# Optimization experiments

Measured on AMD Instinct MI355X. Metric: run time of the kernel, lower is better.

## Reference

```python
import jax, jax.numpy as jnp
import numpy as np
from jax import lax

T = 256   # sequence length (hard-coded in source: tiled to 256 chars)
L = 128   # num_layers of each GRU stack


def _gru_stack(seq, w_ih, w_hh, b_ih, b_hh):
    """Multi-layer GRU with input_size=hidden_size=1 (torch gate order r,z,n).

    seq:  [T] scalar sequence (feature dim squeezed since H=in=1)
    w_ih, w_hh, b_ih, b_hh: [L, 3] stacked per-layer scalar weights/biases
    returns (out_seq [T], h_n [L])
    """
    def layer(carry_seq, params):
        wi, wh, bi, bh = params  # each [3]
        def step(h, xt):
            gi = wi * xt + bi            # [3] input gates
            gh = wh * h + bh             # [3] hidden gates
            r = jax.nn.sigmoid(gi[0] + gh[0])
            z = jax.nn.sigmoid(gi[1] + gh[1])
            n = jnp.tanh(gi[2] + r * gh[2])
            h_new = (1.0 - z) * n + z * h
            return h_new, h_new
        hT, out = lax.scan(step, jnp.zeros((), carry_seq.dtype), carry_seq)
        return out, hT
    out_seq, h_stack = lax.scan(layer, seq, (w_ih, w_hh, b_ih, b_hh))
    return out_seq, h_stack


def setup_inputs() -> dict:
    key = jax.random.key(0)
    ks = jax.random.split(key, 9)
    # torch GRU init: U(-1/sqrt(H), 1/sqrt(H)) = U(-1, 1) since H=1
    mk = lambda k: jax.random.uniform(k, (L, 3), jnp.float32, -1.0, 1.0)
    return {
        "X": jax.random.normal(ks[0], (T, 1), jnp.float32),
        "enc_w_ih": mk(ks[1]), "enc_w_hh": mk(ks[2]),
        "enc_b_ih": mk(ks[3]), "enc_b_hh": mk(ks[4]),
        "dec_w_ih": mk(ks[5]), "dec_w_hh": mk(ks[6]),
        "dec_b_ih": mk(ks[7]), "dec_b_hh": mk(ks[8]),
    }


def reference(X, enc_w_ih, enc_w_hh, enc_b_ih, enc_b_hh,
              dec_w_ih, dec_w_hh, dec_b_ih, dec_b_hh):
    seq = X[:, 0]  # [T]
    enc_out, _ = _gru_stack(seq, enc_w_ih, enc_w_hh, enc_b_ih, enc_b_hh)
    dec_out, dec_h = _gru_stack(enc_out, dec_w_ih, dec_w_hh, dec_b_ih, dec_b_hh)
    # training-mode return: decoder (output [T,1], h_n [L,1])
    return dec_out[:, None], dec_h[:, None]
```

## Files before the change

### kernel.cpp

```cpp
#include <hip/hip_runtime.h>


#define T_LEN 256
#define MBOX  320
typedef unsigned long long u64;
typedef unsigned int u32;

__device__ __forceinline__ float fexp2(float x) { return __builtin_amdgcn_exp2f(x); }
__device__ __forceinline__ float frcp(float x)  { return __builtin_amdgcn_rcpf(x); }

struct CellW {
    float wri, wrh, brc;
    float wzi, wzh, bzc;
    float wni, bni;
    float wnh, bnh;
};

__device__ __forceinline__ float cell_step(const CellW& c, float x, float h) {
    const float xr  = __builtin_fmaf(c.wri, x, c.brc);
    const float xz  = __builtin_fmaf(c.wzi, x, c.bzc);
    const float gin = __builtin_fmaf(c.wni, x, c.bni);
    const float ghn = __builtin_fmaf(c.wnh, h, c.bnh);
    const float er  = fexp2(__builtin_fmaf(c.wrh, h, xr));
    const float ez  = fexp2(__builtin_fmaf(c.wzh, h, xz));
    const float r   = frcp(1.0f + er);
    const float z   = frcp(1.0f + ez);
    const float en  = fexp2(__builtin_fmaf(r, ghn, gin));
    const float q   = frcp(1.0f + en);
    const float A   = __builtin_fmaf(z, h - 1.0f, 1.0f);
    const float B   = __builtin_fmaf(2.0f, z, -2.0f);
    return __builtin_fmaf(q, B, A);
}

template<bool LAST>
__device__ __forceinline__ float run_wave(
    const int j, const CellW& c,
    volatile u64* inbox, volatile u64* outbox,
    float* __restrict__ out, float* __restrict__ dumpG)
{
    float h = 0.0f;
    float hc_prev = 0.0f;
    u32 coll = 0;
    const int js = j & 7;

    {
        u64 v = inbox[8];
        while (__ballot((u32)(v >> 32) == 9u) != ~0ull) v = inbox[8];
    }

    for (int s0 = 0; s0 < 320; s0 += 8) {
        u32 bval = 0;
        if (s0 < T_LEN) {
            const int slot = s0 + js;
            u64 v = inbox[slot];
            while (__ballot((u32)(v >> 32) == (u32)(slot + 1)) != ~0ull)
                v = inbox[slot];
            bval = (u32)v;
        }
        #pragma unroll
        for (int si = 0; si < 8; ++si) {
            const int s = s0 + si;
            const int xv = __builtin_amdgcn_readlane((int)bval, si);
            const int xm = __builtin_amdgcn_update_dpp(
                xv, __builtin_bit_cast(int, hc_prev),
                0x138 , 0xF, 0xF, false);
            const float x = __builtin_bit_cast(float, xm);

            const float hc = cell_step(c, x, h);
            const int t = s - j;
            h = ((u32)t < (u32)T_LEN) ? hc : h;
            hc_prev = hc;

            const int cs = __builtin_amdgcn_update_dpp(
                0, (int)coll, 0x130 , 0xF, 0xF, false);
            coll = (j == 63) ? __builtin_bit_cast(u32, h) : (u32)cs;

            if (si == 6) {
                const int  tm   = s + j - 126;
                const bool real = (j >= 56) & (tm >= 0);
                const int  widx = real ? tm : (T_LEN + j);
                outbox[widx] = ((u64)(u32)(tm + 1) << 32) | (u64)coll;
                if (LAST) {
                    float* p = real ? (out + tm) : (dumpG + j);
                    *p = __builtin_bit_cast(float, coll);
                }
            }
        }
    }
    return h;
}

__global__ __launch_bounds__(256, 1) void gru_pipe8(
    const float* __restrict__ X,
    const float* __restrict__ enc_w_ih, const float* __restrict__ enc_w_hh,
    const float* __restrict__ enc_b_ih, const float* __restrict__ enc_b_hh,
    const float* __restrict__ dec_w_ih, const float* __restrict__ dec_w_hh,
    const float* __restrict__ dec_b_ih, const float* __restrict__ dec_b_hh,
    float* __restrict__ out, float* __restrict__ dumpG)
{
    const int tid = threadIdx.x;
    const int w   = tid >> 6;
    const int j   = tid & 63;

    __shared__ u64 xsM[T_LEN];
    __shared__ u64 box[4][MBOX];

    xsM[tid] = ((u64)(u32)(tid + 1) << 32) |
               (u64)__builtin_bit_cast(u32, X[tid]);
    box[0][tid] = 0ull;
    box[1][tid] = 0ull;
    box[2][tid] = 0ull;
    box[3][tid] = 0ull;

    const int pl = tid & 127;
    const float* wip = (tid < 128) ? enc_w_ih : dec_w_ih;
    const float* whp = (tid < 128) ? enc_w_hh : dec_w_hh;
    const float* bip = (tid < 128) ? enc_b_ih : dec_b_ih;
    const float* bhp = (tid < 128) ? enc_b_hh : dec_b_hh;
    const float L2E = 1.44269504088896340736f;
    CellW c;
    c.wri = -L2E * wip[3 * pl + 0];
    c.wrh = -L2E * whp[3 * pl + 0];
    c.brc = -L2E * (bip[3 * pl + 0] + bhp[3 * pl + 0]);
    c.wzi = -L2E * wip[3 * pl + 1];
    c.wzh = -L2E * whp[3 * pl + 1];
    c.bzc = -L2E * (bip[3 * pl + 1] + bhp[3 * pl + 1]);
    c.wni = 2.0f * L2E * wip[3 * pl + 2];
    c.bni = 2.0f * L2E * bip[3 * pl + 2];
    c.wnh = 2.0f * L2E * whp[3 * pl + 2];
    c.bnh = 2.0f * L2E * bhp[3 * pl + 2];

    __syncthreads();

    volatile u64* inbox  = (w == 0) ? xsM : box[w - 1];
    volatile u64* outbox = box[w];

    float h;
    if (w == 3) h = run_wave<true >(j, c, inbox, outbox, out, dumpG);
    else        h = run_wave<false>(j, c, inbox, outbox, out, dumpG);

    if (w >= 2) out[T_LEN + 64 * (w - 2) + j] = h;
}

extern "C" void kernel_launch(void* const* d_in, const int* in_sizes, int n_in,
                              void* d_out, int out_size, void* d_ws, size_t ws_size,
                              hipStream_t stream) {
    const float* X        = (const float*)d_in[0];
    const float* enc_w_ih = (const float*)d_in[1];
    const float* enc_w_hh = (const float*)d_in[2];
    const float* enc_b_ih = (const float*)d_in[3];
    const float* enc_b_hh = (const float*)d_in[4];
    const float* dec_w_ih = (const float*)d_in[5];
    const float* dec_w_hh = (const float*)d_in[6];
    const float* dec_b_ih = (const float*)d_in[7];
    const float* dec_b_hh = (const float*)d_in[8];
    float* out = (float*)d_out;
    float* dumpG = (float*)d_ws;

    gru_pipe8<<<1, 256, 0, stream>>>(X,
                                     enc_w_ih, enc_w_hh, enc_b_ih, enc_b_hh,
                                     dec_w_ih, dec_w_hh, dec_b_ih, dec_b_hh,
                                     out, dumpG);
}
```

Measured before the change: 113.2 us.

## Pack two GRU layers per lane and use two waves instead of four

Each lane now computes two consecutive layers (A and B), so each stack of 128 layers fits in one 64-lane wavefront. The kernel runs with two waves, encoder and decoder, instead of four. This removes two LDS mailbox handoffs between waves. It also prefetches the next inbox batch before the spin-wait. In exchange each step carries a serial chain of two cell evaluations, and the wavefront pipeline is longer (48 batches, skew 2j), so total serial depth per step roughly doubles while inter-wave synchronization halves.

```diff
diff --git a/kernel.cpp b/kernel.cpp
--- a/kernel.cpp
+++ b/kernel.cpp
@@ -2,7 +2,6 @@
 
 
 #define T_LEN 256
-#define MBOX  320
 typedef unsigned long long u64;
 typedef unsigned int u32;
 
@@ -33,64 +32,77 @@
 }
 
 template<bool LAST>
-__device__ __forceinline__ float run_wave(
-    const int j, const CellW& c,
+__device__ __forceinline__ void run_wave2(
+    const int j, const CellW& cA, const CellW& cB,
     volatile u64* inbox, volatile u64* outbox,
-    float* __restrict__ out, float* __restrict__ dumpG)
+    float* __restrict__ out, float* __restrict__ dumpG,
+    float& hA_out, float& hB_out)
 {
-    float h = 0.0f;
-    float hc_prev = 0.0f;
+    float hA = 0.0f, hB = 0.0f;
+    float hcA_prev = 0.0f, hcB_prev = 0.0f;
     u32 coll = 0;
     const int js = j & 7;
 
     {
-        u64 v = inbox[8];
-        while (__ballot((u32)(v >> 32) == 9u) != ~0ull) v = inbox[8];
+        u64 v = inbox[31];
+        while (__ballot((u32)(v >> 32) == 32u) != ~0ull) v = inbox[31];
     }
+    u64 bnext = inbox[js];
 
-    for (int s0 = 0; s0 < 320; s0 += 8) {
+    #pragma unroll 1
+    for (int b = 0; b < 48; ++b) {
+        const int s0 = b * 8;
         u32 bval = 0;
         if (s0 < T_LEN) {
             const int slot = s0 + js;
-            u64 v = inbox[slot];
+            u64 v = bnext;
             while (__ballot((u32)(v >> 32) == (u32)(slot + 1)) != ~0ull)
                 v = inbox[slot];
             bval = (u32)v;
+            if (s0 + 8 < T_LEN) bnext = inbox[s0 + 8 + js];
         }
         #pragma unroll
         for (int si = 0; si < 8; ++si) {
-            const int s = s0 + si;
-            const int xv = __builtin_amdgcn_readlane((int)bval, si);
+            const int i = s0 + si;
+            const int fv = __builtin_amdgcn_readlane((int)bval, si);
             const int xm = __builtin_amdgcn_update_dpp(
-                xv, __builtin_bit_cast(int, hc_prev),
+                fv, __builtin_bit_cast(int, hcB_prev),
                 0x138 , 0xF, 0xF, false);
-            const float x = __builtin_bit_cast(float, xm);
+            const float xA = __builtin_bit_cast(float, xm);
+            const float xB = hcA_prev;
 
-            const float hc = cell_step(c, x, h);
-            const int t = s - j;
-            h = ((u32)t < (u32)T_LEN) ? hc : h;
-            hc_prev = hc;
+            const float hcA = cell_step(cA, xA, hA);
+            const float hcB = cell_step(cB, xB, hB);
+
+            const int tA = i - 2 * j;
+            const int tB = tA - 1;
+            hA = ((u32)tA < (u32)T_LEN) ? hcA : hA;
+            hB = ((u32)tB < (u32)T_LEN) ? hcB : hB;
+            hcA_prev = hcA;
+            hcB_prev = hcB;
 
             const int cs = __builtin_amdgcn_update_dpp(
                 0, (int)coll, 0x130 , 0xF, 0xF, false);
-            coll = (j == 63) ? __builtin_bit_cast(u32, h) : (u32)cs;
+            coll = (j == 63) ? __builtin_bit_cast(u32, hB) : (u32)cs;
 
             if (si == 6) {
-                const int  tm   = s + j - 126;
+                const int  tm   = i + j - 190;
                 const bool real = (j >= 56) & (tm >= 0);
-                const int  widx = real ? tm : (T_LEN + j);
-                outbox[widx] = ((u64)(u32)(tm + 1) << 32) | (u64)coll;
-                if (LAST) {
+                if (!LAST) {
+                    const int widx = real ? tm : (T_LEN + j);
+                    outbox[widx] = ((u64)(u32)(tm + 1) << 32) | (u64)coll;
+                } else {
                     float* p = real ? (out + tm) : (dumpG + j);
                     *p = __builtin_bit_cast(float, coll);
                 }
             }
         }
     }
-    return h;
+    hA_out = hA;
+    hB_out = hB;
 }
 
-__global__ __launch_bounds__(256, 1) void gru_pipe8(
+__global__ __launch_bounds__(128, 1) void gru_pipe9(
     const float* __restrict__ X,
     const float* __restrict__ enc_w_ih, const float* __restrict__ enc_w_hh,
     const float* __restrict__ enc_b_ih, const float* __restrict__ enc_b_hh,
@@ -103,43 +115,47 @@
     const int j   = tid & 63;
 
     __shared__ u64 xsM[T_LEN];
-    __shared__ u64 box[4][MBOX];
+    __shared__ u64 box[T_LEN + 64];
 
-    xsM[tid] = ((u64)(u32)(tid + 1) << 32) |
-               (u64)__builtin_bit_cast(u32, X[tid]);
-    box[0][tid] = 0ull;
-    box[1][tid] = 0ull;
-    box[2][tid] = 0ull;
-    box[3][tid] = 0ull;
+    xsM[tid]       = ((u64)(u32)(tid + 1) << 32) |
+                     (u64)__builtin_bit_cast(u32, X[tid]);
+    xsM[tid + 128] = ((u64)(u32)(tid + 129) << 32) |
+                     (u64)__builtin_bit_cast(u32, X[tid + 128]);
+    box[tid]       = 0ull;
+    box[tid + 128] = 0ull;
 
-    const int pl = tid & 127;
-    const float* wip = (tid < 128) ? enc_w_ih : dec_w_ih;
-    const float* whp = (tid < 128) ? enc_w_hh : dec_w_hh;
-    const float* bip = (tid < 128) ? enc_b_ih : dec_b_ih;
-    const float* bhp = (tid < 128) ? enc_b_hh : dec_b_hh;
+    const float* wip = (w == 0) ? enc_w_ih : dec_w_ih;
+    const float* whp = (w == 0) ? enc_w_hh : dec_w_hh;
+    const float* bip = (w == 0) ? enc_b_ih : dec_b_ih;
+    const float* bhp = (w == 0) ? enc_b_hh : dec_b_hh;
     const float L2E = 1.44269504088896340736f;
-    CellW c;
-    c.wri = -L2E * wip[3 * pl + 0];
-    c.wrh = -L2E * whp[3 * pl + 0];
-    c.brc = -L2E * (bip[3 * pl + 0] + bhp[3 * pl + 0]);
-    c.wzi = -L2E * wip[3 * pl + 1];
-    c.wzh = -L2E * whp[3 * pl + 1];
-    c.bzc = -L2E * (bip[3 * pl + 1] + bhp[3 * pl + 1]);
-    c.wni = 2.0f * L2E * wip[3 * pl + 2];
-    c.bni = 2.0f * L2E * bip[3 * pl + 2];
-    c.wnh = 2.0f * L2E * whp[3 * pl + 2];
-    c.bnh = 2.0f * L2E * bhp[3 * pl + 2];
+
+    CellW cc[2];
+    #pragma unroll
+    for (int k = 0; k < 2; ++k) {
+        const int pl = 2 * j + k;
+        cc[k].wri = -L2E * wip[3 * pl + 0];
+        cc[k].wrh = -L2E * whp[3 * pl + 0];
+        cc[k].brc = -L2E * (bip[3 * pl + 0] + bhp[3 * pl + 0]);
+        cc[k].wzi = -L2E * wip[3 * pl + 1];
+        cc[k].wzh = -L2E * whp[3 * pl + 1];
+        cc[k].bzc = -L2E * (bip[3 * pl + 1] + bhp[3 * pl + 1]);
+        cc[k].wni = 2.0f * L2E * wip[3 * pl + 2];
+        cc[k].bni = 2.0f * L2E * bip[3 * pl + 2];
+        cc[k].wnh = 2.0f * L2E * whp[3 * pl + 2];
+        cc[k].bnh = 2.0f * L2E * bhp[3 * pl + 2];
+    }
 
     __syncthreads();
 
-    volatile u64* inbox  = (w == 0) ? xsM : box[w - 1];
-    volatile u64* outbox = box[w];
-
-    float h;
-    if (w == 3) h = run_wave<true >(j, c, inbox, outbox, out, dumpG);
-    else        h = run_wave<false>(j, c, inbox, outbox, out, dumpG);
-
-    if (w >= 2) out[T_LEN + 64 * (w - 2) + j] = h;
+    float hA, hB;
+    if (w == 0) {
+        run_wave2<false>(j, cc[0], cc[1], xsM, box, out, dumpG, hA, hB);
+    } else {
+        run_wave2<true >(j, cc[0], cc[1], box, box , out, dumpG, hA, hB);
+        out[T_LEN + 2 * j]     = hA;
+        out[T_LEN + 2 * j + 1] = hB;
+    }
 }
 
 extern "C" void kernel_launch(void* const* d_in, const int* in_sizes, int n_in,
@@ -157,7 +173,7 @@
     float* out = (float*)d_out;
     float* dumpG = (float*)d_ws;
 
-    gru_pipe8<<<1, 256, 0, stream>>>(X,
+    gru_pipe9<<<1, 128, 0, stream>>>(X,
                                      enc_w_ih, enc_w_hh, enc_b_ih, enc_b_hh,
                                      dec_w_ih, dec_w_hh, dec_b_ih, dec_b_hh,
                                      out, dumpG);
```

New measurement: 133.6 us. 18.1% more time.

## Split GRU wavefront loop into masked/unmasked phases and publish outbox twice per batch

Applied to the files above, without the earlier changes.

Reorders the cell math so the hidden-state FMAs start before the input arrives, putting the input term last on the critical path. Splits the 40-batch loop into prologue, steady-state and drain phases, so the middle phase skips the validity mask and the drain phase skips inbox polling. Publishes collected outputs at two points per 8-step batch instead of one, so the next wave can start earlier and waits on an earlier slot. The LAST wave no longer writes to an unused LDS outbox. In exchange it adds code size and a tighter cross-wave handshake protocol that must stay consistent.

```diff
diff --git a/kernel.cpp b/kernel.cpp
--- a/kernel.cpp
+++ b/kernel.cpp
@@ -17,12 +17,12 @@
 };
 
 __device__ __forceinline__ float cell_step(const CellW& c, float x, float h) {
-    const float xr  = __builtin_fmaf(c.wri, x, c.brc);
-    const float xz  = __builtin_fmaf(c.wzi, x, c.bzc);
+    const float hr  = __builtin_fmaf(c.wrh, h, c.brc);
+    const float hz  = __builtin_fmaf(c.wzh, h, c.bzc);
+    const float ghn = __builtin_fmaf(c.wnh, h, c.bnh);
     const float gin = __builtin_fmaf(c.wni, x, c.bni);
-    const float ghn = __builtin_fmaf(c.wnh, h, c.bnh);
-    const float er  = fexp2(__builtin_fmaf(c.wrh, h, xr));
-    const float ez  = fexp2(__builtin_fmaf(c.wzh, h, xz));
+    const float er  = fexp2(__builtin_fmaf(c.wri, x, hr));
+    const float ez  = fexp2(__builtin_fmaf(c.wzi, x, hz));
     const float r   = frcp(1.0f + er);
     const float z   = frcp(1.0f + ez);
     const float en  = fexp2(__builtin_fmaf(r, ghn, gin));
@@ -32,65 +32,85 @@
     return __builtin_fmaf(q, B, A);
 }
 
+template<bool MASKED, bool READ, bool LAST>
+__device__ __forceinline__ void do_batch(
+    const int s0, const int j, const int js, const CellW& c,
+    volatile u64* inbox, volatile u64* outbox,
+    float* __restrict__ out, float* __restrict__ dumpG,
+    float& h, float& hcp, u32& coll)
+{
+    u32 bval = 0;
+    if (READ) {
+        const int slot = s0 + js;
+        u64 v = inbox[slot];
+        while (__ballot((u32)(v >> 32) == (u32)(slot + 1)) != ~0ull)
+            v = inbox[slot];
+        bval = (u32)v;
+    }
+    #pragma unroll
+    for (int si = 0; si < 8; ++si) {
+        const int s = s0 + si;
+        const int fv = READ ? __builtin_amdgcn_readlane((int)bval, si) : 0;
+        const int xm = __builtin_amdgcn_update_dpp(
+            fv, __builtin_bit_cast(int, hcp), 0x138 , 0xF, 0xF, false);
+        const float x = __builtin_bit_cast(float, xm);
+
+        const float hc = cell_step(c, x, h);
+        if (MASKED) {
+            const int t = s - j;
+            h = ((u32)t < (u32)T_LEN) ? hc : h;
+        } else {
+            h = hc;
+        }
+        hcp = hc;
+
+        const int cs = __builtin_amdgcn_update_dpp(
+            0, (int)coll, 0x130 , 0xF, 0xF, false);
+        coll = (j == 63) ? __builtin_bit_cast(u32, h) : (u32)cs;
+
+        if (si == 2 || si == 6) {
+            const int  tm   = s + j - 126;
+            const bool real = (j >= 60) & (tm >= 0);
+            if (!LAST) {
+                const int widx = real ? tm : (T_LEN + j);
+                outbox[widx] = ((u64)(u32)(tm + 1) << 32) | (u64)coll;
+            } else {
+                float* p = real ? (out + tm) : (dumpG + j);
+                *p = __builtin_bit_cast(float, coll);
+            }
+        }
+    }
+}
+
 template<bool LAST>
 __device__ __forceinline__ float run_wave(
     const int j, const CellW& c,
     volatile u64* inbox, volatile u64* outbox,
     float* __restrict__ out, float* __restrict__ dumpG)
 {
-    float h = 0.0f;
-    float hc_prev = 0.0f;
+    float h = 0.0f, hcp = 0.0f;
     u32 coll = 0;
     const int js = j & 7;
 
     {
-        u64 v = inbox[8];
-        while (__ballot((u32)(v >> 32) == 9u) != ~0ull) v = inbox[8];
+        u64 v = inbox[11];
+        while (__ballot((u32)(v >> 32) == 12u) != ~0ull) v = inbox[11];
     }
 
-    for (int s0 = 0; s0 < 320; s0 += 8) {
-        u32 bval = 0;
-        if (s0 < T_LEN) {
-            const int slot = s0 + js;
-            u64 v = inbox[slot];
-            while (__ballot((u32)(v >> 32) == (u32)(slot + 1)) != ~0ull)
-                v = inbox[slot];
-            bval = (u32)v;
-        }
-        #pragma unroll
-        for (int si = 0; si < 8; ++si) {
-            const int s = s0 + si;
-            const int xv = __builtin_amdgcn_readlane((int)bval, si);
-            const int xm = __builtin_amdgcn_update_dpp(
-                xv, __builtin_bit_cast(int, hc_prev),
-                0x138 , 0xF, 0xF, false);
-            const float x = __builtin_bit_cast(float, xm);
+    #pragma unroll 1
+    for (int b = 0; b < 8; ++b)
+        do_batch<true, true, LAST>(b * 8, j, js, c, inbox, outbox, out, dumpG, h, hcp, coll);
+    #pragma unroll 1
+    for (int b = 8; b < 32; ++b)
+        do_batch<false, true, LAST>(b * 8, j, js, c, inbox, outbox, out, dumpG, h, hcp, coll);
+    #pragma unroll 1
+    for (int b = 32; b < 40; ++b)
+        do_batch<true, false, LAST>(b * 8, j, js, c, inbox, outbox, out, dumpG, h, hcp, coll);
 
-            const float hc = cell_step(c, x, h);
-            const int t = s - j;
-            h = ((u32)t < (u32)T_LEN) ? hc : h;
-            hc_prev = hc;
-
-            const int cs = __builtin_amdgcn_update_dpp(
-                0, (int)coll, 0x130 , 0xF, 0xF, false);
-            coll = (j == 63) ? __builtin_bit_cast(u32, h) : (u32)cs;
-
-            if (si == 6) {
-                const int  tm   = s + j - 126;
-                const bool real = (j >= 56) & (tm >= 0);
-                const int  widx = real ? tm : (T_LEN + j);
-                outbox[widx] = ((u64)(u32)(tm + 1) << 32) | (u64)coll;
-                if (LAST) {
-                    float* p = real ? (out + tm) : (dumpG + j);
-                    *p = __builtin_bit_cast(float, coll);
-                }
-            }
-        }
-    }
     return h;
 }
 
-__global__ __launch_bounds__(256, 1) void gru_pipe8(
+__global__ __launch_bounds__(256, 1) void gru_pipe10(
     const float* __restrict__ X,
     const float* __restrict__ enc_w_ih, const float* __restrict__ enc_w_hh,
     const float* __restrict__ enc_b_ih, const float* __restrict__ enc_b_hh,
@@ -157,8 +177,8 @@
     float* out = (float*)d_out;
     float* dumpG = (float*)d_ws;
 
-    gru_pipe8<<<1, 256, 0, stream>>>(X,
-                                     enc_w_ih, enc_w_hh, enc_b_ih, enc_b_hh,
-                                     dec_w_ih, dec_w_hh, dec_b_ih, dec_b_hh,
-                                     out, dumpG);
+    gru_pipe10<<<1, 256, 0, stream>>>(X,
+                                      enc_w_ih, enc_w_hh, enc_b_ih, enc_b_hh,
+                                      dec_w_ih, dec_w_hh, dec_b_ih, dec_b_hh,
+                                      out, dumpG);
 }
```

New measurement: 107.6 us. 1.05x faster.
